# Optimization experiments

Hardware: AMD Instinct MI355X
Metric: run time of the kernel (lower is better)

## Reference

```python
import jax, jax.numpy as jnp
import numpy as np

N_NODES = 100000
DROP_P = 0.2


def _degree_norm(idx, n):
    deg = jax.ops.segment_sum(jnp.ones_like(idx, dtype=jnp.float32), idx, num_segments=n)
    return jnp.maximum(deg, 1.0) ** -0.5


def gcn_layer(x, src, dst, W, b, n):
    # DGL GraphConv, norm='both', in_feats > out_feats so weight is applied first.
    norm_src = _degree_norm(src, n)  # out-degree^{-1/2}
    norm_dst = _degree_norm(dst, n)  # in-degree^{-1/2}
    h = (x * norm_src[:, None]) @ W            # [N, d_out]
    agg = jax.ops.segment_sum(h[src], dst, num_segments=n)  # gather-scatter over edges
    return agg * norm_dst[:, None] + b


def setup_inputs() -> dict:
    key = jax.random.key(0)
    k = jax.random.split(key, 5)
    x = jax.random.normal(k[0], (N_NODES, 256), dtype=jnp.float32)
    edge_index = jax.random.randint(k[1], (2, 1600000), 0, N_NODES, dtype=jnp.int64)
    W1 = jax.random.normal(k[2], (256, 128), dtype=jnp.float32) * (1.0 / np.sqrt(256))
    b1 = jnp.zeros((128,), dtype=jnp.float32)
    W2 = jax.random.normal(k[3], (128, 47), dtype=jnp.float32) * (1.0 / np.sqrt(128))
    b2 = jnp.zeros((47,), dtype=jnp.float32)
    return {"x": x, "edge_index": edge_index, "W1": W1, "b1": b1, "W2": W2, "b2": b2}


def reference(x, edge_index, W1, b1, W2, b2):
    src, dst = edge_index[0], edge_index[1]
    n = x.shape[0]
    # CRD: GraphConv -> relu -> dropout (F.dropout default training=True; fixed mask)
    h = gcn_layer(x, src, dst, W1, b1, n)
    h = jax.nn.relu(h)
    keep = jax.random.bernoulli(jax.random.key(42), 1.0 - DROP_P, h.shape)
    h = jnp.where(keep, h / (1.0 - DROP_P), 0.0)
    # CLS: GraphConv -> log_softmax over class dim
    out = gcn_layer(h, src, dst, W2, b2, n)
    return jax.nn.log_softmax(out, axis=-1)
```

## Files before the change

### kernel.cpp

```cpp
#include <hip/hip_runtime.h>
#include <math.h>


#define NF0 256
#define NF1 128
#define NC  47
#define CB  1024

typedef __attribute__((ext_vector_type(8))) short bfrag;
typedef __attribute__((ext_vector_type(4))) float f32x4;

__device__ __forceinline__ unsigned short f2bf(float f) {
  unsigned u = __float_as_uint(f);
  return (unsigned short)((u + 0x7fffu + ((u >> 16) & 1u)) >> 16);
}
__device__ __forceinline__ unsigned pack2bf(float a, float b) {
  return (unsigned)f2bf(a) | ((unsigned)f2bf(b) << 16);
}
__device__ __forceinline__ float bflo(unsigned v) { return __uint_as_float(v << 16); }
__device__ __forceinline__ float bfhi(unsigned v) { return __uint_as_float(v & 0xffff0000u); }
__device__ __forceinline__ float bf2f(unsigned short b) {
  return __uint_as_float((unsigned)b << 16);
}

__device__ __forceinline__ unsigned rotl_(unsigned x, int n) {
  return (x << n) | (x >> (32 - n));
}
__device__ __forceinline__ void threefry2x32_(unsigned x0, unsigned x1,
                                              unsigned& o0, unsigned& o1) {
  const unsigned k0 = 0u, k1 = 42u;
  const unsigned k2 = k0 ^ k1 ^ 0x1BD11BDAu;
  x0 += k0; x1 += k1;
  x0+=x1; x1=rotl_(x1,13); x1^=x0;
  x0+=x1; x1=rotl_(x1,15); x1^=x0;
  x0+=x1; x1=rotl_(x1,26); x1^=x0;
  x0+=x1; x1=rotl_(x1, 6); x1^=x0;
  x0+=k1; x1+=k2+1u;
  x0+=x1; x1=rotl_(x1,17); x1^=x0;
  x0+=x1; x1=rotl_(x1,29); x1^=x0;
  x0+=x1; x1=rotl_(x1,16); x1^=x0;
  x0+=x1; x1=rotl_(x1,24); x1^=x0;
  x0+=k2; x1+=k0+2u;
  x0+=x1; x1=rotl_(x1,13); x1^=x0;
  x0+=x1; x1=rotl_(x1,15); x1^=x0;
  x0+=x1; x1=rotl_(x1,26); x1^=x0;
  x0+=x1; x1=rotl_(x1, 6); x1^=x0;
  x0+=k0; x1+=k1+3u;
  x0+=x1; x1=rotl_(x1,17); x1^=x0;
  x0+=x1; x1=rotl_(x1,29); x1^=x0;
  x0+=x1; x1=rotl_(x1,16); x1^=x0;
  x0+=x1; x1=rotl_(x1,24); x1^=x0;
  x0+=k1; x1+=k2+4u;
  x0+=x1; x1=rotl_(x1,13); x1^=x0;
  x0+=x1; x1=rotl_(x1,15); x1^=x0;
  x0+=x1; x1=rotl_(x1,26); x1^=x0;
  x0+=x1; x1=rotl_(x1, 6); x1^=x0;
  x0+=k2; x1+=k0+5u;
  o0 = x0; o1 = x1;
}
__device__ __forceinline__ unsigned dropout_bit(unsigned j) {
  unsigned o0, o1;
  threefry2x32_(0u, j, o0, o1);
  unsigned bits = o0 ^ o1;
  float u = __uint_as_float((bits >> 9) | 0x3f800000u) - 1.0f;
  return (u < 0.8f) ? 1u : 0u;
}

__global__ __launch_bounds__(256) void k_chist(const int* __restrict__ ei, int E,
                                               int nbk,
                                               unsigned* __restrict__ bCntD,
                                               unsigned* __restrict__ srcCnt,
                                               const float* __restrict__ W1,
                                               const float* __restrict__ W2,
                                               unsigned* __restrict__ W1t32,
                                               unsigned* __restrict__ W2t32) {
  if (blockIdx.x >= 256) {
    int i = (blockIdx.x - 256) * 256 + threadIdx.x;
    if (i < 128 * 128) {
      int n = i >> 7, k = (i & 127) << 1;
      W1t32[i] = pack2bf(W1[(size_t)k * NF1 + n], W1[(size_t)(k + 1) * NF1 + n]);
    } else if (i < 128 * 128 + 48 * 64) {
      int j = i - 128 * 128;
      int f = j >> 6, k = (j & 63) << 1;
      float a = (f < NC) ? W2[(size_t)k * NC + f] : 0.f;
      float c = (f < NC) ? W2[(size_t)(k + 1) * NC + f] : 0.f;
      W2t32[j] = pack2bf(a, c);
    }
    return;
  }
  __shared__ unsigned hd[128];
  for (int i = threadIdx.x; i < 128; i += 256) hd[i] = 0;
  __syncthreads();
  for (int e = blockIdx.x * 256 + threadIdx.x; e < E; e += 256 * 256) {
    int s = ei[e], d = ei[E + e];
    atomicAdd(&srcCnt[s], 1u);
    atomicAdd(&hd[d >> 10], 1u);
  }
  __syncthreads();
  for (int i = threadIdx.x; i < nbk; i += 256) {
    if (hd[i]) atomicAdd(&bCntD[i], hd[i]);
  }
}

__global__ __launch_bounds__(256) void k_super(const int* __restrict__ ei, int E,
                                               int nbk, int N, int gblk,
                                               const unsigned* __restrict__ bCntD,
                                               unsigned* __restrict__ curD,
                                               unsigned* __restrict__ pd,
                                               const float* __restrict__ x,
                                               const unsigned* __restrict__ W1t32,
                                               const unsigned* __restrict__ srcCnt,
                                               unsigned short* __restrict__ h1,
                                               unsigned* __restrict__ bmask) {
  __shared__ unsigned smem[2 * 128 * 20];
  const int t = threadIdx.x;

  if ((int)blockIdx.x < 256) {
    unsigned* hd    = smem;
    unsigned* baseD = smem + 128;
    unsigned* sc    = smem + 256;
    const int per = (E + 255) / 256;
    const int e0 = blockIdx.x * per;
    const int e1 = min(e0 + per, E);
    unsigned orig = 0;
    if (t < 128) {
      orig = (t < nbk) ? bCntD[t] : 0u;
      sc[t] = orig;
      hd[t] = 0;
    }
    __syncthreads();
    for (int e = e0 + t; e < e1; e += 256) {
      int d = ei[E + e];
      atomicAdd(&hd[d >> 10], 1u);
    }
    __syncthreads();
    #pragma unroll
    for (int o = 1; o < 128; o <<= 1) {
      unsigned u = (t < 128 && t >= o) ? sc[t - o] : 0u;
      __syncthreads();
      if (t < 128) sc[t] += u;
      __syncthreads();
    }
    if (t < 128) {
      unsigned excl = sc[t] - orig;
      unsigned h = hd[t];
      baseD[t] = excl + (h ? atomicAdd(&curD[t], h) : 0u);
      hd[t] = 0;
    }
    __syncthreads();
    for (int e = e0 + t; e < e1; e += 256) {
      int s = ei[e], d = ei[E + e];
      int bd = d >> 10;
      unsigned pD = baseD[bd] + atomicAdd(&hd[bd], 1u);
      pd[pD] = ((unsigned)(d & (CB - 1)) << 17) | (unsigned)s;
    }
    return;
  }

  if ((int)blockIdx.x < 256 + gblk) {
    unsigned (*As)[20] = (unsigned(*)[20])smem;
    unsigned (*Bs)[20] = (unsigned(*)[20])(smem + 128 * 20);
    const int m0 = ((int)blockIdx.x - 256) * 128;
    const int lane = t & 63, wid = t >> 6;
    const int fr = lane & 15, ko = (lane >> 4) * 8;

    f32x4 acc[2][8];
    #pragma unroll
    for (int r = 0; r < 2; r++)
      #pragma unroll
      for (int c = 0; c < 8; c++) acc[r][c] = (f32x4){0.f, 0.f, 0.f, 0.f};

    const int sr = t >> 1;
    const int shw = (t & 1) * 8;

    for (int k0 = 0; k0 < NF0; k0 += 32) {
      {
        unsigned w[8];
        int gm = m0 + sr;
        if (gm < N) {
          const float* p = x + (size_t)gm * NF0 + k0 + shw * 2;
          #pragma unroll
          for (int q = 0; q < 4; q++) {
            float4 v = *(const float4*)(p + q * 4);
            w[2*q]   = pack2bf(v.x, v.y);
            w[2*q+1] = pack2bf(v.z, v.w);
          }
        } else {
          #pragma unroll
          for (int q = 0; q < 8; q++) w[q] = 0u;
        }
        *(uint4*)&As[sr][shw]     = make_uint4(w[0], w[1], w[2], w[3]);
        *(uint4*)&As[sr][shw + 4] = make_uint4(w[4], w[5], w[6], w[7]);
      }
      {
        const unsigned* pb = W1t32 + (size_t)sr * (NF0 / 2) + (k0 >> 1) + shw;
        *(uint4*)&Bs[sr][shw]     = *(const uint4*)pb;
        *(uint4*)&Bs[sr][shw + 4] = *(const uint4*)(pb + 4);
      }
      __syncthreads();
      const unsigned short* As16 = (const unsigned short*)smem;
      const unsigned short* Bs16 = (const unsigned short*)(smem + 128 * 20);
      #pragma unroll
      for (int r = 0; r < 2; r++) {
        bfrag a = *(const bfrag*)(As16 + (size_t)(wid * 32 + r * 16 + fr) * 40 + ko);
        #pragma unroll
        for (int c = 0; c < 8; c++) {
          bfrag b = *(const bfrag*)(Bs16 + (size_t)(c * 16 + fr) * 40 + ko);
          acc[r][c] = __builtin_amdgcn_mfma_f32_16x16x32_bf16(a, b, acc[r][c], 0, 0, 0);
        }
      }
      __syncthreads();
    }

    #pragma unroll
    for (int r = 0; r < 2; r++) {
      int rbase = m0 + wid * 32 + r * 16 + (lane >> 4) * 4;
      float ns[4];
      #pragma unroll
      for (int g = 0; g < 4; g++) {
        int row = rbase + g;
        if (row < N) {
          unsigned c = srcCnt[row];
          ns[g] = 1.0f / sqrtf((float)(c < 1u ? 1u : c));
        } else ns[g] = 0.f;
      }
      #pragma unroll
      for (int c = 0; c < 8; c++) {
        int col = c * 16 + fr;
        #pragma unroll
        for (int g = 0; g < 4; g++) {
          int row = rbase + g;
          if (row < N) h1[(size_t)row * NF1 + col] = f2bf(acc[r][c][g] * ns[g]);
        }
      }
    }
    return;
  }

  int i = ((int)blockIdx.x - 256 - gblk) * 256 + t;
  if (i < 4 * N) {
    unsigned w = 0;
    #pragma unroll 4
    for (int tbit = 0; tbit < 32; tbit++)
      w |= dropout_bit(32u * (unsigned)i + (unsigned)tbit) << tbit;
    bmask[i] = w;
  }
}

__global__ __launch_bounds__(256) void k_fine(const unsigned* __restrict__ bCntD,
                                              const unsigned* __restrict__ pd,
                                              unsigned* __restrict__ off,
                                              float* __restrict__ norm_dst,
                                              int* __restrict__ csr,
                                              int N, int E, int nbk) {
  __shared__ unsigned cnt[CB];
  __shared__ unsigned part[256];
  __shared__ unsigned sc[128];
  const int t = threadIdx.x;
  const int b = blockIdx.x;
  unsigned orig = 0;
  if (t < 128) {
    orig = (t < nbk) ? bCntD[t] : 0u;
    sc[t] = orig;
  }
  __syncthreads();
  #pragma unroll
  for (int o = 1; o < 128; o <<= 1) {
    unsigned u = (t < 128 && t >= o) ? sc[t - o] : 0u;
    __syncthreads();
    if (t < 128) sc[t] += u;
    __syncthreads();
  }
  const unsigned hi = sc[b];
  const unsigned lo = hi - bCntD[b];
  const int base = b << 10;
  for (int i = t; i < CB; i += 256) cnt[i] = 0;
  __syncthreads();
  for (unsigned j = lo + t; j < hi; j += 256) atomicAdd(&cnt[pd[j] >> 17], 1u);
  __syncthreads();
  unsigned c0 = cnt[4*t], c1 = cnt[4*t+1], c2 = cnt[4*t+2], c3 = cnt[4*t+3];
  unsigned tsum = c0 + c1 + c2 + c3;
  part[t] = tsum;
  __syncthreads();
  #pragma unroll
  for (int o = 1; o < 256; o <<= 1) {
    unsigned u = (t >= o) ? part[t - o] : 0u;
    __syncthreads();
    part[t] += u;
    __syncthreads();
  }
  unsigned e0 = part[t] - tsum;
  unsigned p0 = e0, p1 = e0 + c0, p2 = p1 + c1, p3 = p2 + c2;
  int n0 = base + 4 * t;
  if (n0 + 0 < N) { off[n0+0] = lo + p0; norm_dst[n0+0] = 1.0f / sqrtf((float)(c0 < 1u ? 1u : c0)); }
  if (n0 + 1 < N) { off[n0+1] = lo + p1; norm_dst[n0+1] = 1.0f / sqrtf((float)(c1 < 1u ? 1u : c1)); }
  if (n0 + 2 < N) { off[n0+2] = lo + p2; norm_dst[n0+2] = 1.0f / sqrtf((float)(c2 < 1u ? 1u : c2)); }
  if (n0 + 3 < N) { off[n0+3] = lo + p3; norm_dst[n0+3] = 1.0f / sqrtf((float)(c3 < 1u ? 1u : c3)); }
  if (b == nbk - 1 && t == 0) off[N] = (unsigned)E;
  __syncthreads();
  cnt[4*t] = p0; cnt[4*t+1] = p1; cnt[4*t+2] = p2; cnt[4*t+3] = p3;
  __syncthreads();
  for (unsigned j = lo + t; j < hi; j += 256) {
    unsigned v = pd[j];
    unsigned pos = atomicAdd(&cnt[v >> 17], 1u);
    csr[lo + pos] = (int)(v & 0x1FFFFu);
  }
}

__global__ __launch_bounds__(256) void k_gather1(const unsigned* __restrict__ off,
                                                 const int* __restrict__ csr,
                                                 const unsigned short* __restrict__ h1,
                                                 const float* __restrict__ norm_dst,
                                                 const unsigned* __restrict__ srcCnt,
                                                 const float* __restrict__ b1,
                                                 const unsigned* __restrict__ bmask,
                                                 const unsigned* __restrict__ W2t32,
                                                 unsigned short* __restrict__ g64,
                                                 int N) {
  const int t = threadIdx.x;
  const int lane = t & 63, wid = t >> 6;
  const int eg = lane >> 4;
  const int q  = lane & 15;
  const float4 bA = *(const float4*)(b1 + q * 8);
  const float4 bB = *(const float4*)(b1 + q * 8 + 4);

  const int wbase = (blockIdx.x * 4 + wid) * 16;
  if (wbase >= N) return;

  uint4 af[4];
  #pragma unroll
  for (int kk = 0; kk < 4; kk++) af[kk] = make_uint4(0u, 0u, 0u, 0u);

  #pragma unroll 1
  for (int i = 0; i < 16; i++) {
    const int node = wbase + i;
    if (node >= N) break;
    unsigned j = off[node], e1 = off[node + 1];
    float ax0=0.f, ax1=0.f, ax2=0.f, ax3=0.f;
    float ay0=0.f, ay1=0.f, ay2=0.f, ay3=0.f;
    for (; j + 8 <= e1; j += 8) {
      int sA = csr[j + eg];
      int sB = csr[j + 4 + eg];
      uint4 vA = *(const uint4*)(h1 + (size_t)sA * NF1 + q * 8);
      uint4 vB = *(const uint4*)(h1 + (size_t)sB * NF1 + q * 8);
      ax0 += bflo(vA.x) + bflo(vB.x); ay0 += bfhi(vA.x) + bfhi(vB.x);
      ax1 += bflo(vA.y) + bflo(vB.y); ay1 += bfhi(vA.y) + bfhi(vB.y);
      ax2 += bflo(vA.z) + bflo(vB.z); ay2 += bfhi(vA.z) + bfhi(vB.z);
      ax3 += bflo(vA.w) + bflo(vB.w); ay3 += bfhi(vA.w) + bfhi(vB.w);
    }
    if (j + 4 <= e1) {
      int s = csr[j + eg];
      uint4 v = *(const uint4*)(h1 + (size_t)s * NF1 + q * 8);
      ax0 += bflo(v.x); ay0 += bfhi(v.x);
      ax1 += bflo(v.y); ay1 += bfhi(v.y);
      ax2 += bflo(v.z); ay2 += bfhi(v.z);
      ax3 += bflo(v.w); ay3 += bfhi(v.w);
      j += 4;
    }
    if (j < e1) {
      unsigned rem = e1 - j;
      if ((unsigned)eg < rem) {
        int s = csr[j + eg];
        uint4 v = *(const uint4*)(h1 + (size_t)s * NF1 + q * 8);
        ax0 += bflo(v.x); ay0 += bfhi(v.x);
        ax1 += bflo(v.y); ay1 += bfhi(v.y);
        ax2 += bflo(v.z); ay2 += bfhi(v.z);
        ax3 += bflo(v.w); ay3 += bfhi(v.w);
      }
    }
    ax0 += __shfl_xor(ax0, 16); ax0 += __shfl_xor(ax0, 32);
    ay0 += __shfl_xor(ay0, 16); ay0 += __shfl_xor(ay0, 32);
    ax1 += __shfl_xor(ax1, 16); ax1 += __shfl_xor(ax1, 32);
    ay1 += __shfl_xor(ay1, 16); ay1 += __shfl_xor(ay1, 32);
    ax2 += __shfl_xor(ax2, 16); ax2 += __shfl_xor(ax2, 32);
    ay2 += __shfl_xor(ay2, 16); ay2 += __shfl_xor(ay2, 32);
    ax3 += __shfl_xor(ax3, 16); ax3 += __shfl_xor(ax3, 32);
    ay3 += __shfl_xor(ay3, 16); ay3 += __shfl_xor(ay3, 32);
    float nd = norm_dst[node];
    unsigned sc = srcCnt[node];
    float ns = 1.0f / sqrtf((float)(sc < 1u ? 1u : sc));
    unsigned mw = bmask[node * 4 + (q >> 2)];
    unsigned mb = (mw >> ((q & 3) * 8)) & 0xffu;
    float v0 = fmaxf(ax0 * nd + bA.x, 0.f);
    float v1 = fmaxf(ay0 * nd + bA.y, 0.f);
    float v2 = fmaxf(ax1 * nd + bA.z, 0.f);
    float v3 = fmaxf(ay1 * nd + bA.w, 0.f);
    float v4 = fmaxf(ax2 * nd + bB.x, 0.f);
    float v5 = fmaxf(ay2 * nd + bB.y, 0.f);
    float v6 = fmaxf(ax3 * nd + bB.z, 0.f);
    float v7 = fmaxf(ay3 * nd + bB.w, 0.f);
    v0 *= ((mb >> 0) & 1 ? 1.25f : 0.f) * ns;
    v1 *= ((mb >> 1) & 1 ? 1.25f : 0.f) * ns;
    v2 *= ((mb >> 2) & 1 ? 1.25f : 0.f) * ns;
    v3 *= ((mb >> 3) & 1 ? 1.25f : 0.f) * ns;
    v4 *= ((mb >> 4) & 1 ? 1.25f : 0.f) * ns;
    v5 *= ((mb >> 5) & 1 ? 1.25f : 0.f) * ns;
    v6 *= ((mb >> 6) & 1 ? 1.25f : 0.f) * ns;
    v7 *= ((mb >> 7) & 1 ? 1.25f : 0.f) * ns;
    uint4 o;
    o.x = pack2bf(v0, v1);
    o.y = pack2bf(v2, v3);
    o.z = pack2bf(v4, v5);
    o.w = pack2bf(v6, v7);
    #pragma unroll
    for (int kk = 0; kk < 4; kk++) {
      int srcl = 4 * kk + eg;
      unsigned t0 = __shfl(o.x, srcl);
      unsigned t1 = __shfl(o.y, srcl);
      unsigned t2 = __shfl(o.z, srcl);
      unsigned t3 = __shfl(o.w, srcl);
      if (q == i) af[kk] = make_uint4(t0, t1, t2, t3);
    }
  }

  #pragma unroll
  for (int c = 0; c < 3; c++) {
    f32x4 acc = (f32x4){0.f, 0.f, 0.f, 0.f};
    const unsigned* bp = W2t32 + (size_t)(c * 16 + q) * 64 + eg * 4;
    #pragma unroll
    for (int kk = 0; kk < 4; kk++) {
      uint4 w = *(const uint4*)(bp + kk * 16);
      acc = __builtin_amdgcn_mfma_f32_16x16x32_bf16(*(bfrag*)&af[kk], *(bfrag*)&w,
                                                    acc, 0, 0, 0);
    }
    int col = c * 16 + q;
    #pragma unroll
    for (int r = 0; r < 4; r++) {
      int nr = wbase + eg * 4 + r;
      if (nr < N) g64[(size_t)nr * 64 + col] = f2bf(acc[r]);
    }
  }
  #pragma unroll
  for (int r = 0; r < 4; r++) {
    int nr = wbase + eg * 4 + r;
    if (nr < N) g64[(size_t)nr * 64 + 48 + q] = 0;
  }
}

__global__ __launch_bounds__(256) void k_gather2(const unsigned* __restrict__ off,
                                                 const int* __restrict__ csr,
                                                 const unsigned* __restrict__ g64,
                                                 const float* __restrict__ norm_dst,
                                                 const float* __restrict__ b2,
                                                 float* __restrict__ out, int N) {
  int node = (blockIdx.x * 256 + threadIdx.x) >> 6;
  int lane = threadIdx.x & 63;
  if (node >= N) return;
  const int h = lane >> 5, q = lane & 31;
  unsigned j = off[node], e1 = off[node + 1];
  float a0 = 0.f, a1 = 0.f;
  for (; j + 8 <= e1; j += 8) {
    int s0 = csr[j + h],     s1 = csr[j + 2 + h];
    int s2 = csr[j + 4 + h], s3 = csr[j + 6 + h];
    unsigned v0 = g64[(size_t)s0 * 32 + q];
    unsigned v1 = g64[(size_t)s1 * 32 + q];
    unsigned v2 = g64[(size_t)s2 * 32 + q];
    unsigned v3 = g64[(size_t)s3 * 32 + q];
    a0 += (bflo(v0) + bflo(v1)) + (bflo(v2) + bflo(v3));
    a1 += (bfhi(v0) + bfhi(v1)) + (bfhi(v2) + bfhi(v3));
  }
  if (j + 4 <= e1) {
    int sA = csr[j + h], sB = csr[j + 2 + h];
    unsigned vA = g64[(size_t)sA * 32 + q];
    unsigned vB = g64[(size_t)sB * 32 + q];
    a0 += bflo(vA) + bflo(vB);
    a1 += bfhi(vA) + bfhi(vB);
    j += 4;
  }
  if (j + 2 <= e1) {
    int s = csr[j + h];
    unsigned v = g64[(size_t)s * 32 + q];
    a0 += bflo(v); a1 += bfhi(v);
    j += 2;
  }
  if (j < e1 && h == 0) {
    int s = csr[j];
    unsigned v = g64[(size_t)s * 32 + q];
    a0 += bflo(v); a1 += bfhi(v);
  }
  a0 += __shfl_xor(a0, 32);
  a1 += __shfl_xor(a1, 32);
  float nd = norm_dst[node];
  int f0 = 2 * q, f1 = 2 * q + 1;
  float v0 = (f0 < NC) ? a0 * nd + b2[f0] : -INFINITY;
  float v1 = (f1 < NC) ? a1 * nd + b2[f1] : -INFINITY;
  float m = fmaxf(v0, v1);
  #pragma unroll
  for (int o = 16; o; o >>= 1) m = fmaxf(m, __shfl_xor(m, o));
  float ex = ((f0 < NC) ? expf(v0 - m) : 0.f) + ((f1 < NC) ? expf(v1 - m) : 0.f);
  #pragma unroll
  for (int o = 16; o; o >>= 1) ex += __shfl_xor(ex, o);
  float ls = logf(ex);
  if (h == 0) {
    if (f0 < NC) out[(size_t)node * NC + f0] = v0 - m - ls;
    if (f1 < NC) out[(size_t)node * NC + f1] = v1 - m - ls;
  }
}

extern "C" void kernel_launch(void* const* d_in, const int* in_sizes, int n_in,
                              void* d_out, int out_size, void* d_ws, size_t ws_size,
                              hipStream_t stream) {
  const float* x  = (const float*)d_in[0];
  const int*   ei = (const int*)d_in[1];
  const float* W1 = (const float*)d_in[2];
  const float* b1 = (const float*)d_in[3];
  const float* W2 = (const float*)d_in[4];
  const float* b2 = (const float*)d_in[5];
  float* out = (float*)d_out;

  const int N = in_sizes[0] / NF0;
  const int E = in_sizes[1] / 2;
  const int nbk = (N + CB - 1) / CB;
  const int Npad = (N + 63) & ~63;

  unsigned* ws = (unsigned*)d_ws;
  size_t o = 0;
  auto alloc = [&](size_t elems) { size_t p = o; o += (elems + 3) & ~(size_t)3; return p; };
  float*    norm_dst = (float*)(ws + alloc(N));
  unsigned* off      = ws + alloc(N + 1);
  unsigned* bCntD    = ws + alloc(128);
  unsigned* curD     = ws + alloc(128);
  unsigned* srcCnt   = ws + alloc(N);
  unsigned* bmask    = ws + alloc((size_t)4 * N);
  unsigned* pd       = ws + alloc(E);
  int*      csr      = (int*)(ws + alloc(E));
  unsigned* W1t32    = ws + alloc(128 * 128);
  unsigned* W2t32    = ws + alloc(48 * 64);
  unsigned short* h1 = (unsigned short*)(ws + alloc((size_t)N * NF1 / 2));
  unsigned* g64u     = ws + alloc((size_t)Npad * 32);
  unsigned short* g64 = (unsigned short*)g64u;

  hipMemsetAsync(bCntD, 0, (size_t)(256 + N) * sizeof(unsigned), stream);

  int wblk = (128 * 128 + 48 * 64 + 255) / 256;
  int gblk = (N + 127) / 128;
  int mblk = (4 * N + 255) / 256;
  k_chist<<<256 + wblk, 256, 0, stream>>>(ei, E, nbk, bCntD, srcCnt, W1, W2,
                                          W1t32, W2t32);
  k_super<<<256 + gblk + mblk, 256, 0, stream>>>(ei, E, nbk, N, gblk, bCntD, curD,
                                                 pd, x, W1t32, srcCnt, h1, bmask);
  k_fine<<<nbk, 256, 0, stream>>>(bCntD, pd, off, norm_dst, csr, N, E, nbk);
  k_gather1<<<(N + 63) / 64, 256, 0, stream>>>(off, csr, h1, norm_dst, srcCnt,
                                               b1, bmask, W2t32, g64, N);
  k_gather2<<<((size_t)N * 64 + 255) / 256, 256, 0, stream>>>(
      off, csr, (const unsigned*)g64u, norm_dst, b2, out, N);
}
```

Baseline: 472.7 us.

## Replace two-level bucketed CSR build with direct per-node counts and atomic scatter

Builds the CSR by counting per-destination degrees in the histogram kernel, scanning them into offsets, and scattering sources directly with per-node global atomics. This drops the intermediate bucketed pd array and its second pass. The dropout mask generation moves into the histogram kernel, and the GEMM becomes its own kernel. It trades the fused k_super launch for more launches and heavier global atomic traffic, and neighbor order within each row becomes nondeterministic.

```diff
diff --git a/kernel.cpp b/kernel.cpp
--- a/kernel.cpp
+++ b/kernel.cpp
@@ -6,7 +6,6 @@
 #define NF1 128
 #define NC  47
 #define CB  1024
-
 typedef __attribute__((ext_vector_type(8))) short bfrag;
 typedef __attribute__((ext_vector_type(4))) float f32x4;
 
@@ -19,9 +18,6 @@
 }
 __device__ __forceinline__ float bflo(unsigned v) { return __uint_as_float(v << 16); }
 __device__ __forceinline__ float bfhi(unsigned v) { return __uint_as_float(v & 0xffff0000u); }
-__device__ __forceinline__ float bf2f(unsigned short b) {
-  return __uint_as_float((unsigned)b << 16);
-}
 
 __device__ __forceinline__ unsigned rotl_(unsigned x, int n) {
   return (x << n) | (x >> (32 - n));
@@ -67,15 +63,29 @@
 }
 
 __global__ __launch_bounds__(256) void k_chist(const int* __restrict__ ei, int E,
-                                               int nbk,
+                                               int nbk, int N, int wblk,
                                                unsigned* __restrict__ bCntD,
                                                unsigned* __restrict__ srcCnt,
+                                               unsigned* __restrict__ dstCnt,
                                                const float* __restrict__ W1,
                                                const float* __restrict__ W2,
                                                unsigned* __restrict__ W1t32,
-                                               unsigned* __restrict__ W2t32) {
+                                               unsigned* __restrict__ W2t32,
+                                               unsigned* __restrict__ bmask) {
+  const int t = threadIdx.x;
+  if ((int)blockIdx.x >= 256 + wblk) {
+    int i = ((int)blockIdx.x - 256 - wblk) * 256 + t;
+    if (i < 4 * N) {
+      unsigned w = 0;
+      #pragma unroll 4
+      for (int tbit = 0; tbit < 32; tbit++)
+        w |= dropout_bit(32u * (unsigned)i + (unsigned)tbit) << tbit;
+      bmask[i] = w;
+    }
+    return;
+  }
   if (blockIdx.x >= 256) {
-    int i = (blockIdx.x - 256) * 256 + threadIdx.x;
+    int i = (blockIdx.x - 256) * 256 + t;
     if (i < 128 * 128) {
       int n = i >> 7, k = (i & 127) << 1;
       W1t32[i] = pack2bf(W1[(size_t)k * NF1 + n], W1[(size_t)(k + 1) * NF1 + n]);
@@ -89,173 +99,28 @@
     return;
   }
   __shared__ unsigned hd[128];
-  for (int i = threadIdx.x; i < 128; i += 256) hd[i] = 0;
+  for (int i = t; i < 128; i += 256) hd[i] = 0;
   __syncthreads();
-  for (int e = blockIdx.x * 256 + threadIdx.x; e < E; e += 256 * 256) {
+  for (int e = blockIdx.x * 256 + t; e < E; e += 256 * 256) {
     int s = ei[e], d = ei[E + e];
     atomicAdd(&srcCnt[s], 1u);
+    atomicAdd(&dstCnt[d], 1u);
     atomicAdd(&hd[d >> 10], 1u);
   }
   __syncthreads();
-  for (int i = threadIdx.x; i < nbk; i += 256) {
+  for (int i = t; i < nbk; i += 256) {
     if (hd[i]) atomicAdd(&bCntD[i], hd[i]);
   }
 }
 
-__global__ __launch_bounds__(256) void k_super(const int* __restrict__ ei, int E,
-                                               int nbk, int N, int gblk,
-                                               const unsigned* __restrict__ bCntD,
-                                               unsigned* __restrict__ curD,
-                                               unsigned* __restrict__ pd,
-                                               const float* __restrict__ x,
-                                               const unsigned* __restrict__ W1t32,
-                                               const unsigned* __restrict__ srcCnt,
-                                               unsigned short* __restrict__ h1,
-                                               unsigned* __restrict__ bmask) {
-  __shared__ unsigned smem[2 * 128 * 20];
-  const int t = threadIdx.x;
-
-  if ((int)blockIdx.x < 256) {
-    unsigned* hd    = smem;
-    unsigned* baseD = smem + 128;
-    unsigned* sc    = smem + 256;
-    const int per = (E + 255) / 256;
-    const int e0 = blockIdx.x * per;
-    const int e1 = min(e0 + per, E);
-    unsigned orig = 0;
-    if (t < 128) {
-      orig = (t < nbk) ? bCntD[t] : 0u;
-      sc[t] = orig;
-      hd[t] = 0;
-    }
-    __syncthreads();
-    for (int e = e0 + t; e < e1; e += 256) {
-      int d = ei[E + e];
-      atomicAdd(&hd[d >> 10], 1u);
-    }
-    __syncthreads();
-    #pragma unroll
-    for (int o = 1; o < 128; o <<= 1) {
-      unsigned u = (t < 128 && t >= o) ? sc[t - o] : 0u;
-      __syncthreads();
-      if (t < 128) sc[t] += u;
-      __syncthreads();
-    }
-    if (t < 128) {
-      unsigned excl = sc[t] - orig;
-      unsigned h = hd[t];
-      baseD[t] = excl + (h ? atomicAdd(&curD[t], h) : 0u);
-      hd[t] = 0;
-    }
-    __syncthreads();
-    for (int e = e0 + t; e < e1; e += 256) {
-      int s = ei[e], d = ei[E + e];
-      int bd = d >> 10;
-      unsigned pD = baseD[bd] + atomicAdd(&hd[bd], 1u);
-      pd[pD] = ((unsigned)(d & (CB - 1)) << 17) | (unsigned)s;
-    }
-    return;
-  }
-
-  if ((int)blockIdx.x < 256 + gblk) {
-    unsigned (*As)[20] = (unsigned(*)[20])smem;
-    unsigned (*Bs)[20] = (unsigned(*)[20])(smem + 128 * 20);
-    const int m0 = ((int)blockIdx.x - 256) * 128;
-    const int lane = t & 63, wid = t >> 6;
-    const int fr = lane & 15, ko = (lane >> 4) * 8;
-
-    f32x4 acc[2][8];
-    #pragma unroll
-    for (int r = 0; r < 2; r++)
-      #pragma unroll
-      for (int c = 0; c < 8; c++) acc[r][c] = (f32x4){0.f, 0.f, 0.f, 0.f};
-
-    const int sr = t >> 1;
-    const int shw = (t & 1) * 8;
-
-    for (int k0 = 0; k0 < NF0; k0 += 32) {
-      {
-        unsigned w[8];
-        int gm = m0 + sr;
-        if (gm < N) {
-          const float* p = x + (size_t)gm * NF0 + k0 + shw * 2;
-          #pragma unroll
-          for (int q = 0; q < 4; q++) {
-            float4 v = *(const float4*)(p + q * 4);
-            w[2*q]   = pack2bf(v.x, v.y);
-            w[2*q+1] = pack2bf(v.z, v.w);
-          }
-        } else {
-          #pragma unroll
-          for (int q = 0; q < 8; q++) w[q] = 0u;
-        }
-        *(uint4*)&As[sr][shw]     = make_uint4(w[0], w[1], w[2], w[3]);
-        *(uint4*)&As[sr][shw + 4] = make_uint4(w[4], w[5], w[6], w[7]);
-      }
-      {
-        const unsigned* pb = W1t32 + (size_t)sr * (NF0 / 2) + (k0 >> 1) + shw;
-        *(uint4*)&Bs[sr][shw]     = *(const uint4*)pb;
-        *(uint4*)&Bs[sr][shw + 4] = *(const uint4*)(pb + 4);
-      }
-      __syncthreads();
-      const unsigned short* As16 = (const unsigned short*)smem;
-      const unsigned short* Bs16 = (const unsigned short*)(smem + 128 * 20);
-      #pragma unroll
-      for (int r = 0; r < 2; r++) {
-        bfrag a = *(const bfrag*)(As16 + (size_t)(wid * 32 + r * 16 + fr) * 40 + ko);
-        #pragma unroll
-        for (int c = 0; c < 8; c++) {
-          bfrag b = *(const bfrag*)(Bs16 + (size_t)(c * 16 + fr) * 40 + ko);
-          acc[r][c] = __builtin_amdgcn_mfma_f32_16x16x32_bf16(a, b, acc[r][c], 0, 0, 0);
-        }
-      }
-      __syncthreads();
-    }
-
-    #pragma unroll
-    for (int r = 0; r < 2; r++) {
-      int rbase = m0 + wid * 32 + r * 16 + (lane >> 4) * 4;
-      float ns[4];
-      #pragma unroll
-      for (int g = 0; g < 4; g++) {
-        int row = rbase + g;
-        if (row < N) {
-          unsigned c = srcCnt[row];
-          ns[g] = 1.0f / sqrtf((float)(c < 1u ? 1u : c));
-        } else ns[g] = 0.f;
-      }
-      #pragma unroll
-      for (int c = 0; c < 8; c++) {
-        int col = c * 16 + fr;
-        #pragma unroll
-        for (int g = 0; g < 4; g++) {
-          int row = rbase + g;
-          if (row < N) h1[(size_t)row * NF1 + col] = f2bf(acc[r][c][g] * ns[g]);
-        }
-      }
-    }
-    return;
-  }
-
-  int i = ((int)blockIdx.x - 256 - gblk) * 256 + t;
-  if (i < 4 * N) {
-    unsigned w = 0;
-    #pragma unroll 4
-    for (int tbit = 0; tbit < 32; tbit++)
-      w |= dropout_bit(32u * (unsigned)i + (unsigned)tbit) << tbit;
-    bmask[i] = w;
-  }
-}
-
-__global__ __launch_bounds__(256) void k_fine(const unsigned* __restrict__ bCntD,
-                                              const unsigned* __restrict__ pd,
+__global__ __launch_bounds__(256) void k_scan(const unsigned* __restrict__ bCntD,
+                                              const unsigned* __restrict__ dstCnt,
                                               unsigned* __restrict__ off,
                                               float* __restrict__ norm_dst,
-                                              int* __restrict__ csr,
                                               int N, int E, int nbk) {
-  __shared__ unsigned cnt[CB];
+  __shared__ unsigned sc[128];
   __shared__ unsigned part[256];
-  __shared__ unsigned sc[128];
+  __shared__ unsigned cpreS;
   const int t = threadIdx.x;
   const int b = blockIdx.x;
   unsigned orig = 0;
@@ -271,14 +136,15 @@
     if (t < 128) sc[t] += u;
     __syncthreads();
   }
-  const unsigned hi = sc[b];
-  const unsigned lo = hi - bCntD[b];
+  if (t == 0) cpreS = sc[b] - bCntD[b];
+  __syncthreads();
+  const unsigned cpre = cpreS;
   const int base = b << 10;
-  for (int i = t; i < CB; i += 256) cnt[i] = 0;
-  __syncthreads();
-  for (unsigned j = lo + t; j < hi; j += 256) atomicAdd(&cnt[pd[j] >> 17], 1u);
-  __syncthreads();
-  unsigned c0 = cnt[4*t], c1 = cnt[4*t+1], c2 = cnt[4*t+2], c3 = cnt[4*t+3];
+  const int n0 = base + 4 * t;
+  unsigned c0 = (n0 + 0 < N) ? dstCnt[n0 + 0] : 0u;
+  unsigned c1 = (n0 + 1 < N) ? dstCnt[n0 + 1] : 0u;
+  unsigned c2 = (n0 + 2 < N) ? dstCnt[n0 + 2] : 0u;
+  unsigned c3 = (n0 + 3 < N) ? dstCnt[n0 + 3] : 0u;
   unsigned tsum = c0 + c1 + c2 + c3;
   part[t] = tsum;
   __syncthreads();
@@ -291,19 +157,104 @@
   }
   unsigned e0 = part[t] - tsum;
   unsigned p0 = e0, p1 = e0 + c0, p2 = p1 + c1, p3 = p2 + c2;
-  int n0 = base + 4 * t;
-  if (n0 + 0 < N) { off[n0+0] = lo + p0; norm_dst[n0+0] = 1.0f / sqrtf((float)(c0 < 1u ? 1u : c0)); }
-  if (n0 + 1 < N) { off[n0+1] = lo + p1; norm_dst[n0+1] = 1.0f / sqrtf((float)(c1 < 1u ? 1u : c1)); }
-  if (n0 + 2 < N) { off[n0+2] = lo + p2; norm_dst[n0+2] = 1.0f / sqrtf((float)(c2 < 1u ? 1u : c2)); }
-  if (n0 + 3 < N) { off[n0+3] = lo + p3; norm_dst[n0+3] = 1.0f / sqrtf((float)(c3 < 1u ? 1u : c3)); }
+  if (n0 + 0 < N) { off[n0+0] = cpre + p0; norm_dst[n0+0] = 1.0f / sqrtf((float)(c0 < 1u ? 1u : c0)); }
+  if (n0 + 1 < N) { off[n0+1] = cpre + p1; norm_dst[n0+1] = 1.0f / sqrtf((float)(c1 < 1u ? 1u : c1)); }
+  if (n0 + 2 < N) { off[n0+2] = cpre + p2; norm_dst[n0+2] = 1.0f / sqrtf((float)(c2 < 1u ? 1u : c2)); }
+  if (n0 + 3 < N) { off[n0+3] = cpre + p3; norm_dst[n0+3] = 1.0f / sqrtf((float)(c3 < 1u ? 1u : c3)); }
   if (b == nbk - 1 && t == 0) off[N] = (unsigned)E;
-  __syncthreads();
-  cnt[4*t] = p0; cnt[4*t+1] = p1; cnt[4*t+2] = p2; cnt[4*t+3] = p3;
-  __syncthreads();
-  for (unsigned j = lo + t; j < hi; j += 256) {
-    unsigned v = pd[j];
-    unsigned pos = atomicAdd(&cnt[v >> 17], 1u);
-    csr[lo + pos] = (int)(v & 0x1FFFFu);
+}
+
+__global__ __launch_bounds__(256) void k_scatter(const int* __restrict__ ei, int E,
+                                                 const unsigned* __restrict__ off,
+                                                 unsigned* __restrict__ cur0,
+                                                 int* __restrict__ csr) {
+  for (int e = blockIdx.x * 256 + threadIdx.x; e < E; e += gridDim.x * 256) {
+    int s = ei[e], d = ei[E + e];
+    unsigned pos = off[d] + atomicAdd(&cur0[d], 1u);
+    csr[pos] = s;
+  }
+}
+
+__global__ __launch_bounds__(256) void k_gemm1(const float* __restrict__ x,
+                                               const unsigned* __restrict__ W1t32,
+                                               const unsigned* __restrict__ srcCnt,
+                                               unsigned short* __restrict__ h1, int N) {
+  __shared__ unsigned As[128][20];
+  __shared__ unsigned Bs[128][20];
+  const int m0 = blockIdx.x * 128;
+  const int t = threadIdx.x;
+  const int lane = t & 63, wid = t >> 6;
+  const int fr = lane & 15, ko = (lane >> 4) * 8;
+
+  f32x4 acc[2][8];
+  #pragma unroll
+  for (int r = 0; r < 2; r++)
+    #pragma unroll
+    for (int c = 0; c < 8; c++) acc[r][c] = (f32x4){0.f, 0.f, 0.f, 0.f};
+
+  const int sr = t >> 1;
+  const int shw = (t & 1) * 8;
+
+  for (int k0 = 0; k0 < NF0; k0 += 32) {
+    {
+      unsigned w[8];
+      int gm = m0 + sr;
+      if (gm < N) {
+        const float* p = x + (size_t)gm * NF0 + k0 + shw * 2;
+        #pragma unroll
+        for (int q = 0; q < 4; q++) {
+          float4 v = *(const float4*)(p + q * 4);
+          w[2*q]   = pack2bf(v.x, v.y);
+          w[2*q+1] = pack2bf(v.z, v.w);
+        }
+      } else {
+        #pragma unroll
+        for (int q = 0; q < 8; q++) w[q] = 0u;
+      }
+      *(uint4*)&As[sr][shw]     = make_uint4(w[0], w[1], w[2], w[3]);
+      *(uint4*)&As[sr][shw + 4] = make_uint4(w[4], w[5], w[6], w[7]);
+    }
+    {
+      const unsigned* pb = W1t32 + (size_t)sr * (NF0 / 2) + (k0 >> 1) + shw;
+      *(uint4*)&Bs[sr][shw]     = *(const uint4*)pb;
+      *(uint4*)&Bs[sr][shw + 4] = *(const uint4*)(pb + 4);
+    }
+    __syncthreads();
+    const unsigned short* As16 = (const unsigned short*)&As[0][0];
+    const unsigned short* Bs16 = (const unsigned short*)&Bs[0][0];
+    #pragma unroll
+    for (int r = 0; r < 2; r++) {
+      bfrag a = *(const bfrag*)(As16 + (size_t)(wid * 32 + r * 16 + fr) * 40 + ko);
+      #pragma unroll
+      for (int c = 0; c < 8; c++) {
+        bfrag b = *(const bfrag*)(Bs16 + (size_t)(c * 16 + fr) * 40 + ko);
+        acc[r][c] = __builtin_amdgcn_mfma_f32_16x16x32_bf16(a, b, acc[r][c], 0, 0, 0);
+      }
+    }
+    __syncthreads();
+  }
+
+  #pragma unroll
+  for (int r = 0; r < 2; r++) {
+    int rbase = m0 + wid * 32 + r * 16 + (lane >> 4) * 4;
+    float ns[4];
+    #pragma unroll
+    for (int g = 0; g < 4; g++) {
+      int row = rbase + g;
+      if (row < N) {
+        unsigned c = srcCnt[row];
+        ns[g] = 1.0f / sqrtf((float)(c < 1u ? 1u : c));
+      } else ns[g] = 0.f;
+    }
+    #pragma unroll
+    for (int c = 0; c < 8; c++) {
+      int col = c * 16 + fr;
+      #pragma unroll
+      for (int g = 0; g < 4; g++) {
+        int row = rbase + g;
+        if (row < N) h1[(size_t)row * NF1 + col] = f2bf(acc[r][c][g] * ns[g]);
+      }
+    }
   }
 }
 
@@ -519,10 +470,10 @@
   float*    norm_dst = (float*)(ws + alloc(N));
   unsigned* off      = ws + alloc(N + 1);
   unsigned* bCntD    = ws + alloc(128);
-  unsigned* curD     = ws + alloc(128);
   unsigned* srcCnt   = ws + alloc(N);
+  unsigned* dstCnt   = ws + alloc(N);
+  unsigned* cur0     = ws + alloc(N);
   unsigned* bmask    = ws + alloc((size_t)4 * N);
-  unsigned* pd       = ws + alloc(E);
   int*      csr      = (int*)(ws + alloc(E));
   unsigned* W1t32    = ws + alloc(128 * 128);
   unsigned* W2t32    = ws + alloc(48 * 64);
@@ -530,16 +481,16 @@
   unsigned* g64u     = ws + alloc((size_t)Npad * 32);
   unsigned short* g64 = (unsigned short*)g64u;
 
-  hipMemsetAsync(bCntD, 0, (size_t)(256 + N) * sizeof(unsigned), stream);
+  hipMemsetAsync(bCntD, 0, (size_t)(128 + 3 * N) * sizeof(unsigned), stream);
 
   int wblk = (128 * 128 + 48 * 64 + 255) / 256;
-  int gblk = (N + 127) / 128;
   int mblk = (4 * N + 255) / 256;
-  k_chist<<<256 + wblk, 256, 0, stream>>>(ei, E, nbk, bCntD, srcCnt, W1, W2,
-                                          W1t32, W2t32);
-  k_super<<<256 + gblk + mblk, 256, 0, stream>>>(ei, E, nbk, N, gblk, bCntD, curD,
-                                                 pd, x, W1t32, srcCnt, h1, bmask);
-  k_fine<<<nbk, 256, 0, stream>>>(bCntD, pd, off, norm_dst, csr, N, E, nbk);
+  k_chist<<<256 + wblk + mblk, 256, 0, stream>>>(ei, E, nbk, N, wblk, bCntD,
+                                                 srcCnt, dstCnt, W1, W2,
+                                                 W1t32, W2t32, bmask);
+  k_scan<<<nbk, 256, 0, stream>>>(bCntD, dstCnt, off, norm_dst, N, E, nbk);
+  k_scatter<<<1024, 256, 0, stream>>>(ei, E, off, cur0, csr);
+  k_gemm1<<<(N + 127) / 128, 256, 0, stream>>>(x, W1t32, srcCnt, h1, N);
   k_gather1<<<(N + 63) / 64, 256, 0, stream>>>(off, csr, h1, norm_dst, srcCnt,
                                                b1, bmask, W2t32, g64, N);
   k_gather2<<<((size_t)N * 64 + 255) / 256, 256, 0, stream>>>(
```

Measured after the change: 586.3 us. +24.0%, slower.
